# Optimization experiments

Measured on AMD Instinct MI355X. Metric: run time of the kernel, lower is better.

Reference implementation:

```python
import jax, jax.numpy as jnp
import numpy as np

DIM = 512
NUM_HEADS = 8
SR = 2
HEAD_DIM = DIM // NUM_HEADS
SCALE = HEAD_DIM ** -0.5
LN_EPS = 1e-5


def setup_inputs() -> dict:
    key = jax.random.key(0)
    ks = jax.random.split(key, 8)
    B, H, W = 8, 64, 64
    N = H * W
    s = DIM ** -0.5
    x = jax.random.normal(ks[0], (B, N, DIM), dtype=jnp.float32)
    q_w = jax.random.normal(ks[1], (DIM, DIM), dtype=jnp.float32) * s
    kv_w = jax.random.normal(ks[2], (2 * DIM, DIM), dtype=jnp.float32) * s
    proj_w = jax.random.normal(ks[3], (DIM, DIM), dtype=jnp.float32) * s
    proj_b = jnp.zeros((DIM,), dtype=jnp.float32)
    # Conv2d(dim, dim, kernel=sr, stride=sr): OIHW
    sr_w = jax.random.normal(ks[4], (DIM, DIM, SR, SR), dtype=jnp.float32) * (DIM * SR * SR) ** -0.5
    sr_b = jnp.zeros((DIM,), dtype=jnp.float32)
    norm_g = jnp.ones((DIM,), dtype=jnp.float32)
    norm_b = jnp.zeros((DIM,), dtype=jnp.float32)
    return {"x": x, "h": H, "w": W, "q_w": q_w, "kv_w": kv_w,
            "proj_w": proj_w, "proj_b": proj_b, "sr_w": sr_w, "sr_b": sr_b,
            "norm_g": norm_g, "norm_b": norm_b}


def _layernorm(x, g, b):
    mu = jnp.mean(x, axis=-1, keepdims=True)
    var = jnp.var(x, axis=-1, keepdims=True)
    return (x - mu) * jax.lax.rsqrt(var + LN_EPS) * g + b


def reference(x, h, w, q_w, kv_w, proj_w, proj_b, sr_w, sr_b, norm_g, norm_b):
    B, N, C = x.shape
    M, c = NUM_HEADS, HEAD_DIM
    # q projection: [B, N, C] -> [B, M, N, c]
    q = (x @ q_w.T).reshape(B, N, M, c).transpose(0, 2, 1, 3)
    # spatial reduction: conv(kernel=SR, stride=SR) + LayerNorm
    xs = x.reshape(B, h, w, C).transpose(0, 3, 1, 2)  # NCHW
    xs = jax.lax.conv_general_dilated(
        xs, sr_w, window_strides=(SR, SR), padding='VALID',
        dimension_numbers=('NCHW', 'OIHW', 'NCHW')) + sr_b[None, :, None, None]
    h2, w2 = h // SR, w // SR
    xs = xs.reshape(B, C, h2 * w2).transpose(0, 2, 1)  # [B, D, C], D = reduced tokens
    xs = _layernorm(xs, norm_g, norm_b)
    # kv projection: 'b d (a m c) -> a b m d c'
    D = h2 * w2
    kv = (xs @ kv_w.T).reshape(B, D, 2, M, c).transpose(2, 0, 3, 1, 4)
    k, v = kv[0], kv[1]  # [B, M, D, c]
    # attention: scores [B, M, N, D]
    attn = jnp.einsum('bmnc,bmdc->bmnd', q, k) * SCALE
    attn = jax.nn.softmax(attn, axis=-1)
    out = jnp.einsum('bmnd,bmdc->bmnc', attn, v)  # [B, M, N, c]
    out = out.transpose(0, 2, 1, 3).reshape(B, N, C)
    return out @ proj_w.T + proj_b
```

## Files before the change

kernel.cpp:

```cpp
#include <hip/hip_runtime.h>
#include <stdint.h>

typedef unsigned short u16;
typedef unsigned int   u32;

using bf16x8 = __attribute__((ext_vector_type(8))) __bf16;
using f32x4  = __attribute__((ext_vector_type(4))) float;
using f32x16 = __attribute__((ext_vector_type(16))) float;

#define GAS(p) ((const __attribute__((address_space(1))) void*)(p))
#define LAS(p) ((__attribute__((address_space(3))) void*)(p))

__device__ __forceinline__ u16 f2bf(float f) {
  union { float f; u32 u; } v; v.f = f;
  return (u16)((v.u + 0x7FFFu + ((v.u >> 16) & 1u)) >> 16);
}

__device__ __forceinline__ u32 cvtpk(float lo, float hi) {
  u32 r;
  asm("v_cvt_pk_bf16_f32 %0, %1, %2" : "=v"(r) : "v"(lo), "v"(hi));
  return r;
}

__device__ __forceinline__ void perm32swap(u32& a, u32& b) {
  asm volatile("v_permlane32_swap_b32 %0, %1" : "+v"(a), "+v"(b));
}

__global__ __launch_bounds__(256) void k_cast_x(const float* __restrict__ x,
    u16* __restrict__ xb) {
  int t   = blockIdx.x * 256 + threadIdx.x;
  int row = t >> 6;
  int seg = t & 63;
  const float* src = x + (size_t)row * 512 + seg * 8;
  float4 a = *(const float4*)src;
  float4 b = *(const float4*)(src + 4);
  uint4 pk;
  pk.x = (u32)f2bf(a.x) | ((u32)f2bf(a.y) << 16);
  pk.y = (u32)f2bf(a.z) | ((u32)f2bf(a.w) << 16);
  pk.z = (u32)f2bf(b.x) | ((u32)f2bf(b.y) << 16);
  pk.w = (u32)f2bf(b.z) | ((u32)f2bf(b.w) << 16);
  *(uint4*)(xb + (size_t)row * 512 + seg * 8) = pk;
}

__global__ __launch_bounds__(256) void k_cast_w(const float* __restrict__ qw,
    const float* __restrict__ kvw, const float* __restrict__ pw,
    const float* __restrict__ srw, u16* __restrict__ oqw, u16* __restrict__ okvw,
    u16* __restrict__ opw, u16* __restrict__ osrw) {
  int t = blockIdx.x * 256 + threadIdx.x;
  if (t < 262144) {
    oqw[t] = f2bf(qw[t]);
  } else if (t < 786432) {
    int i = t - 262144; okvw[i] = f2bf(kvw[i]);
  } else if (t < 1048576) {
    int i = t - 786432; opw[i] = f2bf(pw[i]);
  } else {
    int i = t - 1048576;
    int o  = i >> 11;
    int r  = i & 2047;
    int kk = r >> 9;
    int ic = r & 511;
    int ky = kk >> 1, kx = kk & 1;
    osrw[i] = f2bf(srw[(((size_t)o * 512 + ic) * 2 + ky) * 2 + kx]);
  }
}

__global__ __launch_bounds__(256) void k_gemm_conv(const u16* __restrict__ xb,
    const u16* __restrict__ B, float* __restrict__ C, int N, int K) {
  __shared__ u16 lA[2][128 * 32];
  __shared__ u16 lB[2][128 * 32];
  const int tid  = threadIdx.x;
  const int wid  = tid >> 6;
  const int lane = tid & 63;
  const int brow = blockIdx.x * 128;
  const int bcol = blockIdx.y * 128;
  const int wr = (wid >> 1) * 64;
  const int wc = (wid & 1) * 64;

  const int c0 = wid * 2, c1 = c0 + 1;
  const int rl = lane >> 2;
  const int ks = (lane & 3) * 8;
  auto abase = [&](int r) {
    int b2 = r >> 10, pr = r & 1023;
    return xb + ((size_t)b2 * 4096 + (pr >> 5) * 128 + (pr & 31) * 2) * 512 + ks;
  };
  const u16* gA0 = abase(brow + c0 * 16 + rl);
  const u16* gA1 = abase(brow + c1 * 16 + rl);
  const u16* gB0 = B + (size_t)(bcol + c0 * 16 + rl) * K + ks;
  const u16* gB1 = B + (size_t)(bcol + c1 * 16 + rl) * K + ks;

  f32x4 acc[4][4] = {};
  const int ar = lane & 15;
  const int ak = (lane >> 4) * 8;

  auto stage = [&](int k0, int buf) {
    int off = ((k0 >> 10) & 1) * 32768 + ((k0 >> 9) & 1) * 512 + (k0 & 511);
    __builtin_amdgcn_global_load_lds(GAS(gA0 + off), LAS(&lA[buf][c0 * 512]), 16, 0, 0);
    __builtin_amdgcn_global_load_lds(GAS(gA1 + off), LAS(&lA[buf][c1 * 512]), 16, 0, 0);
    __builtin_amdgcn_global_load_lds(GAS(gB0 + k0),  LAS(&lB[buf][c0 * 512]), 16, 0, 0);
    __builtin_amdgcn_global_load_lds(GAS(gB1 + k0),  LAS(&lB[buf][c1 * 512]), 16, 0, 0);
  };

  stage(0, 0);
  __syncthreads();

  const int nk = K >> 5;
  for (int t = 0; t < nk; ++t) {
    const int buf = t & 1;
    if (t + 1 < nk) stage((t + 1) << 5, buf ^ 1);
    bf16x8 af[4], bfr[4];
#pragma unroll
    for (int m = 0; m < 4; ++m)
      af[m] = *(const bf16x8*)&lA[buf][(wr + m * 16 + ar) * 32 + ak];
#pragma unroll
    for (int n = 0; n < 4; ++n)
      bfr[n] = *(const bf16x8*)&lB[buf][(wc + n * 16 + ar) * 32 + ak];
#pragma unroll
    for (int m = 0; m < 4; ++m)
#pragma unroll
      for (int n = 0; n < 4; ++n)
        acc[m][n] = __builtin_amdgcn_mfma_f32_16x16x32_bf16(af[m], bfr[n], acc[m][n], 0, 0, 0);
    __syncthreads();
  }

  const int crow = brow + wr + (lane >> 4) * 4;
  const int ccol = bcol + wc + (lane & 15);
#pragma unroll
  for (int n = 0; n < 4; ++n) {
    int col = ccol + n * 16;
#pragma unroll
    for (int m = 0; m < 4; ++m)
#pragma unroll
      for (int r = 0; r < 4; ++r)
        C[(size_t)(crow + m * 16 + r) * N + col] = acc[m][n][r];
  }
}

template<bool OUT_BF16, bool ADD_BIAS>
__global__ __launch_bounds__(512) void k_gemm_bt2(const u16* __restrict__ A,
    const u16* __restrict__ B, void* __restrict__ Cv,
    const float* __restrict__ bias, float scale, int M, int N, int K) {
  __shared__ u16 lA[2][256 * 32];
  __shared__ u16 lB[2][128 * 32];
  const int tid  = threadIdx.x;
  const int wid  = tid >> 6;
  const int lane = tid & 63;
  const int brow = blockIdx.x * 256;
  const int bcol = blockIdx.y * 128;
  const int wr = (wid >> 1) * 64;
  const int wc = (wid & 1) * 64;

  const int rl = lane >> 2;
  const int ks = (lane & 3) * 8;
  const u16* gA0 = A + (size_t)(brow + wid * 16 + rl) * K + ks;
  const u16* gA1 = A + (size_t)(brow + 128 + wid * 16 + rl) * K + ks;
  const u16* gB0 = B + (size_t)(bcol + wid * 16 + rl) * K + ks;

  f32x4 acc[4][4] = {};
  const int ar = lane & 15;
  const int ak = (lane >> 4) * 8;

  auto stage = [&](int k0, int buf) {
    __builtin_amdgcn_global_load_lds(GAS(gA0 + k0), LAS(&lA[buf][wid * 512]), 16, 0, 0);
    __builtin_amdgcn_global_load_lds(GAS(gA1 + k0), LAS(&lA[buf][4096 + wid * 512]), 16, 0, 0);
    __builtin_amdgcn_global_load_lds(GAS(gB0 + k0), LAS(&lB[buf][wid * 512]), 16, 0, 0);
  };

  stage(0, 0);
  __syncthreads();

  const int nk = K >> 5;
  for (int t = 0; t < nk; ++t) {
    const int buf = t & 1;
    if (t + 1 < nk) stage((t + 1) << 5, buf ^ 1);
    bf16x8 af[4], bfr[4];
#pragma unroll
    for (int m = 0; m < 4; ++m)
      af[m] = *(const bf16x8*)&lA[buf][(wr + m * 16 + ar) * 32 + ak];
#pragma unroll
    for (int n = 0; n < 4; ++n)
      bfr[n] = *(const bf16x8*)&lB[buf][(wc + n * 16 + ar) * 32 + ak];
#pragma unroll
    for (int m = 0; m < 4; ++m)
#pragma unroll
      for (int n = 0; n < 4; ++n)
        acc[m][n] = __builtin_amdgcn_mfma_f32_16x16x32_bf16(af[m], bfr[n], acc[m][n], 0, 0, 0);
    __syncthreads();
  }

  const int crow = brow + wr + (lane >> 4) * 4;
  const int ccol = bcol + wc + (lane & 15);
#pragma unroll
  for (int n = 0; n < 4; ++n) {
    int col = ccol + n * 16;
    float bv = ADD_BIAS ? bias[col] : 0.0f;
#pragma unroll
    for (int m = 0; m < 4; ++m)
#pragma unroll
      for (int r = 0; r < 4; ++r) {
        size_t idx = (size_t)(crow + m * 16 + r) * N + col;
        float val = acc[m][n][r] * scale + bv;
        if (OUT_BF16) ((u16*)Cv)[idx] = f2bf(val);
        else          ((float*)Cv)[idx] = val;
      }
  }
}

__global__ __launch_bounds__(512) void k_gemm_kv(const u16* __restrict__ A,
    const u16* __restrict__ B, u16* __restrict__ kpk, u16* __restrict__ vpk) {
  const int K = 512;
  __shared__ u16 lA[2][256 * 32];
  __shared__ u16 lB[2][128 * 32];
  const int tid  = threadIdx.x;
  const int wid  = tid >> 6;
  const int lane = tid & 63;
  const int brow = blockIdx.x * 256;
  const int bcol = blockIdx.y * 128;
  const int wr = (wid >> 1) * 64;
  const int wc = (wid & 1) * 64;

  const int rl = lane >> 2;
  const int ks = (lane & 3) * 8;
  const u16* gA0 = A + (size_t)(brow + wid * 16 + rl) * K + ks;
  const u16* gA1 = A + (size_t)(brow + 128 + wid * 16 + rl) * K + ks;
  const u16* gB0 = B + (size_t)(bcol + wid * 16 + rl) * K + ks;

  f32x4 acc[4][4] = {};
  const int ar = lane & 15;
  const int ak = (lane >> 4) * 8;

  auto stage = [&](int k0, int buf) {
    __builtin_amdgcn_global_load_lds(GAS(gA0 + k0), LAS(&lA[buf][wid * 512]), 16, 0, 0);
    __builtin_amdgcn_global_load_lds(GAS(gA1 + k0), LAS(&lA[buf][4096 + wid * 512]), 16, 0, 0);
    __builtin_amdgcn_global_load_lds(GAS(gB0 + k0), LAS(&lB[buf][wid * 512]), 16, 0, 0);
  };

  stage(0, 0);
  __syncthreads();

  const int nk = K >> 5;
  for (int t = 0; t < nk; ++t) {
    const int buf = t & 1;
    if (t + 1 < nk) stage((t + 1) << 5, buf ^ 1);
    bf16x8 af[4], bfr[4];
#pragma unroll
    for (int m = 0; m < 4; ++m)
      af[m] = *(const bf16x8*)&lA[buf][(wr + m * 16 + ar) * 32 + ak];
#pragma unroll
    for (int n = 0; n < 4; ++n)
      bfr[n] = *(const bf16x8*)&lB[buf][(wc + n * 16 + ar) * 32 + ak];
#pragma unroll
    for (int m = 0; m < 4; ++m)
#pragma unroll
      for (int n = 0; n < 4; ++n)
        acc[m][n] = __builtin_amdgcn_mfma_f32_16x16x32_bf16(af[m], bfr[n], acc[m][n], 0, 0, 0);
    __syncthreads();
  }

  const int crow = brow + wr + (lane >> 4) * 4;
  const int ccol = bcol + wc + (lane & 15);
  const bool isV = (bcol >= 512);
  u16* dst = isV ? vpk : kpk;

  int colt[4];
#pragma unroll
  for (int n = 0; n < 4; ++n) {
    int col = ccol + n * 16;
    int rem = col & 511;
    int m = rem >> 6, c = rem & 63;
    colt[n] = isV ? (m * 65536 + (c >> 5) * 2048 + (c & 31) * 8)
                  : (m * 65536 + (c >> 4) * 512 + ((c >> 3) & 1) * 256 + (c & 7));
  }
#pragma unroll
  for (int mi = 0; mi < 4; ++mi)
#pragma unroll
    for (int r = 0; r < 4; ++r) {
      int row = crow + mi * 16 + r;
      int b2 = row >> 10, d = row & 1023;
      int kt = d >> 6, dl = d & 63;
      int rowt = b2 * 524288 + kt * 4096 +
                 (isV ? ((dl >> 4) * 512 + ((dl >> 3) & 1) * 256 + (dl & 7))
                      : ((dl >> 5) * 2048 + (dl & 31) * 8));
#pragma unroll
      for (int n = 0; n < 4; ++n)
        dst[rowt + colt[n]] = f2bf(acc[mi][n][r]);
    }
}

__global__ __launch_bounds__(256) void k_ln(const float* __restrict__ cin,
    const float* __restrict__ srb, const float* __restrict__ g,
    const float* __restrict__ bb, u16* __restrict__ out) {
  int row  = blockIdx.x * 4 + (threadIdx.x >> 6);
  int lane = threadIdx.x & 63;
  const float* src = cin + (size_t)row * 512 + lane * 8;
  float4 a  = *(const float4*)src;
  float4 b  = *(const float4*)(src + 4);
  float4 s1 = *(const float4*)(srb + lane * 8);
  float4 s2 = *(const float4*)(srb + lane * 8 + 4);
  float v[8] = { a.x + s1.x, a.y + s1.y, a.z + s1.z, a.w + s1.w,
                 b.x + s2.x, b.y + s2.y, b.z + s2.z, b.w + s2.w };
  float sum = 0.f, sq = 0.f;
#pragma unroll
  for (int i = 0; i < 8; ++i) { sum += v[i]; sq += v[i] * v[i]; }
  for (int m = 1; m < 64; m <<= 1) {
    sum += __shfl_xor(sum, m, 64);
    sq  += __shfl_xor(sq,  m, 64);
  }
  float mean = sum * (1.0f / 512.0f);
  float var  = sq * (1.0f / 512.0f) - mean * mean;
  float rstd = rsqrtf(var + 1e-5f);
  float4 g1 = *(const float4*)(g + lane * 8);
  float4 g2 = *(const float4*)(g + lane * 8 + 4);
  float4 b1 = *(const float4*)(bb + lane * 8);
  float4 b2 = *(const float4*)(bb + lane * 8 + 4);
  float gg[8] = { g1.x, g1.y, g1.z, g1.w, g2.x, g2.y, g2.z, g2.w };
  float bv[8] = { b1.x, b1.y, b1.z, b1.w, b2.x, b2.y, b2.z, b2.w };
  uint4 pk;
  u32 w0[8];
#pragma unroll
  for (int i = 0; i < 8; ++i) w0[i] = f2bf((v[i] - mean) * rstd * gg[i] + bv[i]);
  pk.x = w0[0] | (w0[1] << 16);
  pk.y = w0[2] | (w0[3] << 16);
  pk.z = w0[4] | (w0[5] << 16);
  pk.w = w0[6] | (w0[7] << 16);
  *(uint4*)(out + (size_t)row * 512 + lane * 8) = pk;
}

__global__ __launch_bounds__(256) void k_attn(const u16* __restrict__ q,
    const u16* __restrict__ kpk, const u16* __restrict__ vpk,
    u16* __restrict__ out) {
  __shared__ u16 kl[2][4096];
  const int sw   = blockIdx.x;
  const int slot = sw >> 3;
  const int bm   = (sw & 7) * 8 + (slot >> 5);
  const int qx   = slot & 31;
  const int b  = bm >> 3, mm = bm & 7;
  const int wid  = threadIdx.x >> 6;
  const int lane = threadIdx.x & 63;
  const int l31  = lane & 31;
  const int hi   = lane >> 5;
  const int hi8  = hi * 8;
  const int q0   = qx * 128 + wid * 32;

  const u16* qrow = q + (size_t)(b * 4096 + q0 + l31) * 512 + mm * 64 + hi8;
  bf16x8 qf[4];
#pragma unroll
  for (int cs = 0; cs < 4; ++cs) qf[cs] = *(const bf16x8*)(qrow + cs * 16);

  const u16* kp = kpk + (size_t)bm * 65536;
  const u16* vp = vpk + (size_t)bm * 65536;
  const int loff = lane * 8;
  const int c0   = wid * 2;

  union { u32 w[4]; bf16x8 v; } onesu;
  onesu.w[0] = onesu.w[1] = onesu.w[2] = onesu.w[3] = 0x3F803F80u;
  const bf16x8 ones = onesu.v;

  f32x16 o0 = {}, o1 = {}, o2 = {};

  auto stage = [&](int t, int buf) {
    const u16* ks = kp + t * 4096 + c0 * 512 + loff;
    __builtin_amdgcn_global_load_lds(GAS(ks),       LAS(&kl[buf][c0 * 512]),       16, 0, 0);
    __builtin_amdgcn_global_load_lds(GAS(ks + 512), LAS(&kl[buf][c0 * 512 + 512]), 16, 0, 0);
  };

  auto body = [&](int t, int buf) {
    if (t + 1 < 16) stage(t + 1, buf ^ 1);

    const u16* vt = vp + t * 4096 + loff;
    bf16x8 vf[8];
#pragma unroll
    for (int i = 0; i < 8; ++i) vf[i] = *(const bf16x8*)(vt + i * 512);

    bf16x8 kf[8];
#pragma unroll
    for (int i = 0; i < 8; ++i)
      kf[i] = *(const bf16x8*)&kl[buf][i * 512 + loff];

    f32x16 s0 = {}, s1 = {};
    __builtin_amdgcn_s_setprio(1);
#pragma unroll
    for (int cs = 0; cs < 4; ++cs) {
      s0 = __builtin_amdgcn_mfma_f32_32x32x16_bf16(kf[cs],     qf[cs], s0, 0, 0, 0);
      s1 = __builtin_amdgcn_mfma_f32_32x32x16_bf16(kf[4 + cs], qf[cs], s1, 0, 0, 0);
    }
    __builtin_amdgcn_s_setprio(0);

    float pr[2][16];
#pragma unroll
    for (int i = 0; i < 16; ++i) {
      pr[0][i] = __builtin_amdgcn_exp2f(s0[i]);
      pr[1][i] = __builtin_amdgcn_exp2f(s1[i]);
    }

    bf16x8 pa[4];
#pragma unroll
    for (int half = 0; half < 2; ++half)
#pragma unroll
      for (int ks = 0; ks < 2; ++ks) {
        u32 wa = cvtpk(pr[half][ks * 8 + 0], pr[half][ks * 8 + 1]);
        u32 wb = cvtpk(pr[half][ks * 8 + 4], pr[half][ks * 8 + 5]);
        u32 wc = cvtpk(pr[half][ks * 8 + 2], pr[half][ks * 8 + 3]);
        u32 wd = cvtpk(pr[half][ks * 8 + 6], pr[half][ks * 8 + 7]);
        perm32swap(wa, wb);
        perm32swap(wc, wd);
        union { u32 w[4]; bf16x8 v; } uu;
        uu.w[0] = wa; uu.w[1] = wc; uu.w[2] = wb; uu.w[3] = wd;
        pa[half * 2 + ks] = uu.v;
      }

    __builtin_amdgcn_s_setprio(1);
#pragma unroll
    for (int ks = 0; ks < 4; ++ks) {
      o0 = __builtin_amdgcn_mfma_f32_32x32x16_bf16(vf[ks],     pa[ks], o0, 0, 0, 0);
      o1 = __builtin_amdgcn_mfma_f32_32x32x16_bf16(vf[4 + ks], pa[ks], o1, 0, 0, 0);
      o2 = __builtin_amdgcn_mfma_f32_32x32x16_bf16(ones,       pa[ks], o2, 0, 0, 0);
    }
    __builtin_amdgcn_s_setprio(0);
    __syncthreads();
  };

  stage(0, 0);
  __syncthreads();
  for (int t = 0; t < 16; t += 2) {
    body(t, 0);
    body(t + 1, 1);
  }

  float inv = 1.0f / o2[0];
  u16* obase = out + (size_t)(b * 4096 + q0 + l31) * 512 + mm * 64 + hi * 4;
#pragma unroll
  for (int ct = 0; ct < 2; ++ct)
#pragma unroll
    for (int g = 0; g < 4; ++g) {
      ushort4 st;
      st.x = f2bf((ct ? o1[g * 4 + 0] : o0[g * 4 + 0]) * inv);
      st.y = f2bf((ct ? o1[g * 4 + 1] : o0[g * 4 + 1]) * inv);
      st.z = f2bf((ct ? o1[g * 4 + 2] : o0[g * 4 + 2]) * inv);
      st.w = f2bf((ct ? o1[g * 4 + 3] : o0[g * 4 + 3]) * inv);
      *(ushort4*)(obase + ct * 32 + g * 8) = st;
    }
}

extern "C" void kernel_launch(void* const* d_in, const int* in_sizes, int n_in,
                              void* d_out, int out_size, void* d_ws, size_t ws_size,
                              hipStream_t stream) {
  const float* x      = (const float*)d_in[0];
  const float* q_w    = (const float*)d_in[3];
  const float* kv_w   = (const float*)d_in[4];
  const float* proj_w = (const float*)d_in[5];
  const float* proj_b = (const float*)d_in[6];
  const float* sr_w   = (const float*)d_in[7];
  const float* sr_b   = (const float*)d_in[8];
  const float* ng     = (const float*)d_in[9];
  const float* nb     = (const float*)d_in[10];

  char* ws = (char*)d_ws;
  size_t off = 0;
  auto alloc = [&](size_t bytes) {
    char* p = ws + off;
    off += (bytes + 255) & ~(size_t)255;
    return p;
  };
  u16* wq      = (u16*)alloc(512 * 512 * 2);
  u16* wkv     = (u16*)alloc(1024 * 512 * 2);
  u16* wpr     = (u16*)alloc(512 * 512 * 2);
  u16* wsr     = (u16*)alloc(512 * 2048 * 2);
  u16* xb      = (u16*)alloc(33554432);
  u16* qbuf    = (u16*)alloc(33554432);
  u16* xsln    = (u16*)alloc(8388608);
  u16* kpkb    = (u16*)alloc(8388608);
  u16* vpkb    = (u16*)alloc(8388608);
  float* convout = (float*)alloc(16777216);
  u16* attn_o  = xb;

  const float zsc = 0.125f * 1.44269504f;

  k_cast_x<<<8192, 256, 0, stream>>>(x, xb);
  k_cast_w<<<8192, 256, 0, stream>>>(q_w, kv_w, proj_w, sr_w, wq, wkv, wpr, wsr);
  k_gemm_bt2<true,  false><<<dim3(128, 4), 512, 0, stream>>>(xb, wq, qbuf, nullptr, zsc, 32768, 512, 512);
  k_gemm_conv<<<dim3(64, 4), 256, 0, stream>>>(xb, wsr, convout, 512, 2048);
  k_ln<<<2048, 256, 0, stream>>>(convout, sr_b, ng, nb, xsln);
  k_gemm_kv<<<dim3(32, 8), 512, 0, stream>>>(xsln, wkv, kpkb, vpkb);
  k_attn<<<2048, 256, 0, stream>>>(qbuf, kpkb, vpkb, attn_o);
  k_gemm_bt2<false, true><<<dim3(128, 4), 512, 0, stream>>>(attn_o, wpr, (float*)d_out, proj_b, 1.0f, 32768, 512, 512);
}
```

Baseline: 239.4 us.

## Merge cast kernels into one launch and halve conv GEMM row tile

The separate x-cast and weight-cast kernels become one launch, with the block index choosing the work, which saves a kernel launch and the gap between them. The conv GEMM row tile drops from 128 to 64 rows per block, so the grid doubles from 256 to 512 blocks. The aim is to fill the 256 CUs of the MI355X better during the long K=2048 loop. In exchange each block reuses its loaded B tile over fewer rows, so arithmetic intensity falls and B is read from global memory twice as often.

```diff
diff --git a/kernel.cpp b/kernel.cpp
--- a/kernel.cpp
+++ b/kernel.cpp
@@ -26,78 +26,76 @@
   asm volatile("v_permlane32_swap_b32 %0, %1" : "+v"(a), "+v"(b));
 }
 
-__global__ __launch_bounds__(256) void k_cast_x(const float* __restrict__ x,
-    u16* __restrict__ xb) {
-  int t   = blockIdx.x * 256 + threadIdx.x;
-  int row = t >> 6;
-  int seg = t & 63;
-  const float* src = x + (size_t)row * 512 + seg * 8;
-  float4 a = *(const float4*)src;
-  float4 b = *(const float4*)(src + 4);
-  uint4 pk;
-  pk.x = (u32)f2bf(a.x) | ((u32)f2bf(a.y) << 16);
-  pk.y = (u32)f2bf(a.z) | ((u32)f2bf(a.w) << 16);
-  pk.z = (u32)f2bf(b.x) | ((u32)f2bf(b.y) << 16);
-  pk.w = (u32)f2bf(b.z) | ((u32)f2bf(b.w) << 16);
-  *(uint4*)(xb + (size_t)row * 512 + seg * 8) = pk;
-}
-
-__global__ __launch_bounds__(256) void k_cast_w(const float* __restrict__ qw,
+__global__ __launch_bounds__(256) void k_cast(const float* __restrict__ x,
+    u16* __restrict__ xb, const float* __restrict__ qw,
     const float* __restrict__ kvw, const float* __restrict__ pw,
     const float* __restrict__ srw, u16* __restrict__ oqw, u16* __restrict__ okvw,
     u16* __restrict__ opw, u16* __restrict__ osrw) {
-  int t = blockIdx.x * 256 + threadIdx.x;
-  if (t < 262144) {
-    oqw[t] = f2bf(qw[t]);
-  } else if (t < 786432) {
-    int i = t - 262144; okvw[i] = f2bf(kvw[i]);
-  } else if (t < 1048576) {
-    int i = t - 786432; opw[i] = f2bf(pw[i]);
+  const int bid = blockIdx.x;
+  if (bid < 8192) {
+    int t   = bid * 256 + threadIdx.x;
+    int row = t >> 6;
+    int seg = t & 63;
+    const float* src = x + (size_t)row * 512 + seg * 8;
+    float4 a = *(const float4*)src;
+    float4 b = *(const float4*)(src + 4);
+    uint4 pk;
+    pk.x = (u32)f2bf(a.x) | ((u32)f2bf(a.y) << 16);
+    pk.y = (u32)f2bf(a.z) | ((u32)f2bf(a.w) << 16);
+    pk.z = (u32)f2bf(b.x) | ((u32)f2bf(b.y) << 16);
+    pk.w = (u32)f2bf(b.z) | ((u32)f2bf(b.w) << 16);
+    *(uint4*)(xb + (size_t)row * 512 + seg * 8) = pk;
   } else {
-    int i = t - 1048576;
-    int o  = i >> 11;
-    int r  = i & 2047;
-    int kk = r >> 9;
-    int ic = r & 511;
-    int ky = kk >> 1, kx = kk & 1;
-    osrw[i] = f2bf(srw[(((size_t)o * 512 + ic) * 2 + ky) * 2 + kx]);
+    int t = (bid - 8192) * 256 + threadIdx.x;
+    if (t < 262144) {
+      oqw[t] = f2bf(qw[t]);
+    } else if (t < 786432) {
+      int i = t - 262144; okvw[i] = f2bf(kvw[i]);
+    } else if (t < 1048576) {
+      int i = t - 786432; opw[i] = f2bf(pw[i]);
+    } else {
+      int i = t - 1048576;
+      int o  = i >> 11;
+      int r  = i & 2047;
+      int kk = r >> 9;
+      int ic = r & 511;
+      int ky = kk >> 1, kx = kk & 1;
+      osrw[i] = f2bf(srw[(((size_t)o * 512 + ic) * 2 + ky) * 2 + kx]);
+    }
   }
 }
 
 __global__ __launch_bounds__(256) void k_gemm_conv(const u16* __restrict__ xb,
     const u16* __restrict__ B, float* __restrict__ C, int N, int K) {
-  __shared__ u16 lA[2][128 * 32];
+  __shared__ u16 lA[2][64 * 32];
   __shared__ u16 lB[2][128 * 32];
   const int tid  = threadIdx.x;
   const int wid  = tid >> 6;
   const int lane = tid & 63;
-  const int brow = blockIdx.x * 128;
+  const int brow = blockIdx.x * 64;
   const int bcol = blockIdx.y * 128;
-  const int wr = (wid >> 1) * 64;
+  const int wr = (wid >> 1) * 32;
   const int wc = (wid & 1) * 64;
 
-  const int c0 = wid * 2, c1 = c0 + 1;
   const int rl = lane >> 2;
   const int ks = (lane & 3) * 8;
   auto abase = [&](int r) {
     int b2 = r >> 10, pr = r & 1023;
     return xb + ((size_t)b2 * 4096 + (pr >> 5) * 128 + (pr & 31) * 2) * 512 + ks;
   };
-  const u16* gA0 = abase(brow + c0 * 16 + rl);
-  const u16* gA1 = abase(brow + c1 * 16 + rl);
-  const u16* gB0 = B + (size_t)(bcol + c0 * 16 + rl) * K + ks;
-  const u16* gB1 = B + (size_t)(bcol + c1 * 16 + rl) * K + ks;
-
-  f32x4 acc[4][4] = {};
+  const u16* gA0 = abase(brow + wid * 16 + rl);
+  const u16* gB0 = B + (size_t)(bcol + (wid * 2 + 0) * 16 + rl) * K + ks;
+  const u16* gB1 = B + (size_t)(bcol + (wid * 2 + 1) * 16 + rl) * K + ks;
+
+  f32x4 acc[2][4] = {};
   const int ar = lane & 15;
   const int ak = (lane >> 4) * 8;
 
   auto stage = [&](int k0, int buf) {
     int off = ((k0 >> 10) & 1) * 32768 + ((k0 >> 9) & 1) * 512 + (k0 & 511);
-    __builtin_amdgcn_global_load_lds(GAS(gA0 + off), LAS(&lA[buf][c0 * 512]), 16, 0, 0);
-    __builtin_amdgcn_global_load_lds(GAS(gA1 + off), LAS(&lA[buf][c1 * 512]), 16, 0, 0);
-    __builtin_amdgcn_global_load_lds(GAS(gB0 + k0),  LAS(&lB[buf][c0 * 512]), 16, 0, 0);
-    __builtin_amdgcn_global_load_lds(GAS(gB1 + k0),  LAS(&lB[buf][c1 * 512]), 16, 0, 0);
+    __builtin_amdgcn_global_load_lds(GAS(gA0 + off), LAS(&lA[buf][wid * 512]), 16, 0, 0);
+    __builtin_amdgcn_global_load_lds(GAS(gB0 + k0),  LAS(&lB[buf][(wid * 2 + 0) * 512]), 16, 0, 0);
+    __builtin_amdgcn_global_load_lds(GAS(gB1 + k0),  LAS(&lB[buf][(wid * 2 + 1) * 512]), 16, 0, 0);
   };
 
   stage(0, 0);
@@ -107,15 +105,15 @@
   for (int t = 0; t < nk; ++t) {
     const int buf = t & 1;
     if (t + 1 < nk) stage((t + 1) << 5, buf ^ 1);
-    bf16x8 af[4], bfr[4];
-#pragma unroll
-    for (int m = 0; m < 4; ++m)
+    bf16x8 af[2], bfr[4];
+#pragma unroll
+    for (int m = 0; m < 2; ++m)
       af[m] = *(const bf16x8*)&lA[buf][(wr + m * 16 + ar) * 32 + ak];
 #pragma unroll
     for (int n = 0; n < 4; ++n)
       bfr[n] = *(const bf16x8*)&lB[buf][(wc + n * 16 + ar) * 32 + ak];
 #pragma unroll
-    for (int m = 0; m < 4; ++m)
+    for (int m = 0; m < 2; ++m)
 #pragma unroll
       for (int n = 0; n < 4; ++n)
         acc[m][n] = __builtin_amdgcn_mfma_f32_16x16x32_bf16(af[m], bfr[n], acc[m][n], 0, 0, 0);
@@ -128,7 +126,7 @@
   for (int n = 0; n < 4; ++n) {
     int col = ccol + n * 16;
 #pragma unroll
-    for (int m = 0; m < 4; ++m)
+    for (int m = 0; m < 2; ++m)
 #pragma unroll
       for (int r = 0; r < 4; ++r)
         C[(size_t)(crow + m * 16 + r) * N + col] = acc[m][n][r];
@@ -475,10 +473,9 @@
 
   const float zsc = 0.125f * 1.44269504f;
 
-  k_cast_x<<<8192, 256, 0, stream>>>(x, xb);
-  k_cast_w<<<8192, 256, 0, stream>>>(q_w, kv_w, proj_w, sr_w, wq, wkv, wpr, wsr);
+  k_cast<<<16384, 256, 0, stream>>>(x, xb, q_w, kv_w, proj_w, sr_w, wq, wkv, wpr, wsr);
   k_gemm_bt2<true,  false><<<dim3(128, 4), 512, 0, stream>>>(xb, wq, qbuf, nullptr, zsc, 32768, 512, 512);
-  k_gemm_conv<<<dim3(64, 4), 256, 0, stream>>>(xb, wsr, convout, 512, 2048);
+  k_gemm_conv<<<dim3(128, 4), 256, 0, stream>>>(xb, wsr, convout, 512, 2048);
   k_ln<<<2048, 256, 0, stream>>>(convout, sr_b, ng, nb, xsln);
   k_gemm_kv<<<dim3(32, 8), 512, 0, stream>>>(xsln, wkv, kpkb, vpkb);
   k_attn<<<2048, 256, 0, stream>>>(qbuf, kpkb, vpkb, attn_o);
```

Measured after the change: 235.1 us, median of 2. No clear change (-1.8%).
